# Optimization experiments

Measured on AMD Instinct MI355X. Metric: run time of the kernel, lower is better.

Reference implementation:

```python
import jax, jax.numpy as jnp
import numpy as np

D_MODEL = 1024
NUM_HEADS = 16
D_K = D_MODEL // NUM_HEADS
THETA = 10000.0


def apply_rope(x, positions):
    # x: [b, h, s, d_k]; positions: [b, s] int32
    half = D_K // 2
    inv_freq = THETA ** (-jnp.arange(half, dtype=jnp.float32) * 2.0 / D_K)  # [half]
    angles = positions[:, None, :, None].astype(jnp.float32) * inv_freq  # [b,1,s,half]
    cos, sin = jnp.cos(angles), jnp.sin(angles)
    x1 = x[..., 0::2]  # even dims
    x2 = x[..., 1::2]  # odd dims
    out_even = x1 * cos - x2 * sin
    out_odd = x1 * sin + x2 * cos
    # re-interleave
    out = jnp.stack([out_even, out_odd], axis=-1)
    return out.reshape(x.shape)


def setup_inputs() -> dict:
    key = jax.random.key(0)
    ks = jax.random.split(key, 5)
    b, s = 2, 2048
    scale = 0.02
    return {
        "x": jax.random.normal(ks[0], (b, s, D_MODEL), dtype=jnp.float32),
        "Wq": jax.random.normal(ks[1], (D_MODEL, D_MODEL), dtype=jnp.float32) * scale,
        "Wk": jax.random.normal(ks[2], (D_MODEL, D_MODEL), dtype=jnp.float32) * scale,
        "Wv": jax.random.normal(ks[3], (D_MODEL, D_MODEL), dtype=jnp.float32) * scale,
        "Wo": jax.random.normal(ks[4], (D_MODEL, D_MODEL), dtype=jnp.float32) * scale,
    }


def reference(x, Wq, Wk, Wv, Wo):
    b, s, _ = x.shape
    # Linear(d, d) applied as x @ W^T (torch Linear convention, no bias)
    Q = x @ Wq.T
    K = x @ Wk.T
    V = x @ Wv.T
    # split heads: [b, s, h*d] -> [b, h, s, d]
    split = lambda t: t.reshape(b, s, NUM_HEADS, D_K).transpose(0, 2, 1, 3)
    Q, K, V = split(Q), split(K), split(V)
    positions = jnp.broadcast_to(jnp.arange(s, dtype=jnp.int32), (b, s))
    Q = apply_rope(Q, positions)
    K = apply_rope(K, positions)
    scores = jnp.einsum('bhqd,bhkd->bhqk', Q, K) / jnp.sqrt(jnp.float32(D_K))
    causal = jnp.tril(jnp.ones((s, s), dtype=bool))
    scores = jnp.where(causal[None, None], scores, -jnp.inf)
    attn = jax.nn.softmax(scores, axis=-1)
    out = jnp.einsum('bhqk,bhkd->bhqd', attn, V)
    out = out.transpose(0, 2, 1, 3).reshape(b, s, D_MODEL)
    return out @ Wo.T
```

## Files before the change

### kernel.cpp

```cpp
#include <hip/hip_runtime.h>

typedef __attribute__((ext_vector_type(8))) short bf16x8;
typedef __attribute__((ext_vector_type(4))) float f32x4;
typedef __attribute__((ext_vector_type(16))) float f32x16;

typedef const __attribute__((address_space(1))) unsigned int gu32;
typedef __attribute__((address_space(3))) unsigned int lu32;

__device__ __forceinline__ void async16(const void* g, void* l) {
  __builtin_amdgcn_global_load_lds((gu32*)g, (lu32*)l, 16, 0, 0);
}

__device__ __forceinline__ unsigned short f2bf(float f) {
  unsigned int u = __float_as_uint(f);
  u += 0x7fffu + ((u >> 16) & 1u);
  return (unsigned short)(u >> 16);
}
__device__ __forceinline__ float b2f(unsigned short s) {
  return __uint_as_float(((unsigned int)s) << 16);
}
__device__ __forceinline__ unsigned int cvtpk(float lo, float hi) {
  unsigned int w;
  asm("v_cvt_pk_bf16_f32 %0, %1, %2" : "=v"(w) : "v"(lo), "v"(hi));
  return w;
}
__device__ __forceinline__ void plswap(unsigned int& x, unsigned int& y) {
  asm("v_permlane32_swap_b32 %0, %1" : "+v"(x), "+v"(y));
}
__device__ __forceinline__ float max3f(float a, float b, float c) {
  float d;
  asm("v_max3_f32 %0, %1, %2, %3" : "=v"(d) : "v"(a), "v"(b), "v"(c));
  return d;
}

__global__ __launch_bounds__(256) void cvt_all(const float* __restrict__ x,
                                               const float* __restrict__ Wq,
                                               const float* __restrict__ Wk,
                                               const float* __restrict__ Wv,
                                               const float* __restrict__ Wo,
                                               unsigned short* __restrict__ xb,
                                               unsigned short* __restrict__ Wb,
                                               unsigned short* __restrict__ Wob) {
  int i = blockIdx.x * 256 + threadIdx.x;
  const float* src;
  unsigned short* dst;
  int j;
  if (i < (1 << 20)) {
    src = x; dst = xb; j = i;
  } else {
    int k = i - (1 << 20);
    int wsel = k >> 18;
    j = k & 0x3FFFF;
    src = (wsel == 0) ? Wq : (wsel == 1) ? Wk : (wsel == 2) ? Wv : Wo;
    dst = (wsel == 0) ? Wb : (wsel == 1) ? Wb + (1 << 20)
        : (wsel == 2) ? Wb + (2 << 20) : Wob;
  }
  float4 v = ((const float4*)src)[j];
  ushort4 o;
  o.x = f2bf(v.x); o.y = f2bf(v.y); o.z = f2bf(v.z); o.w = f2bf(v.w);
  ((ushort4*)dst)[j] = o;
}

template <int WRITE_F32>
__global__ __launch_bounds__(256) void gemm_bt(const unsigned short* __restrict__ A,
                                               const unsigned short* __restrict__ B,
                                               void* __restrict__ Cp, int N, int K) {
  __shared__ __align__(16) unsigned short Al[3][128 * 32];
  __shared__ __align__(16) unsigned short Bl[3][128 * 32];
  const int t = threadIdx.x;
  const int w = t >> 6, l = t & 63;
  const int wm = w >> 1, wn = w & 1;
  const int lr = l & 15, lg = l >> 4;
  const long bm = (long)blockIdx.x * 128, bn = (long)blockIdx.y * 128;
  const int srow = t >> 2;
  const int c8 = t & 3;
  const int KT = K >> 5;
  f32x4 acc[4][4] = {};

  auto STAGE = [&](int ts) {
    const int bi = ts % 3;
    const int k0 = ts * 32;
    #pragma unroll
    for (int r = 0; r < 2; ++r) {
      int row = r * 64 + srow;
      async16(&A[(bm + row) * (long)K + k0 + c8 * 8], &Al[bi][row * 32 + c8 * 8]);
      async16(&B[(bn + row) * (long)K + k0 + c8 * 8], &Bl[bi][row * 32 + c8 * 8]);
    }
  };

  STAGE(0);
  STAGE(1);
  for (int kt = 0; kt < KT; ++kt) {
    const int cur = kt % 3;
    if (kt < KT - 1) asm volatile("s_waitcnt vmcnt(4)" ::: "memory");
    else             asm volatile("s_waitcnt vmcnt(0)" ::: "memory");
    __builtin_amdgcn_s_barrier();
    __builtin_amdgcn_sched_barrier(0);
    if (kt + 2 < KT) STAGE(kt + 2);
    bf16x8 af[4], bf[4];
    #pragma unroll
    for (int i = 0; i < 4; ++i) {
      af[i] = *(const bf16x8*)&Al[cur][(wm * 64 + i * 16 + lr) * 32 + lg * 8];
      bf[i] = *(const bf16x8*)&Bl[cur][(wn * 64 + i * 16 + lr) * 32 + lg * 8];
    }
    #pragma unroll
    for (int i = 0; i < 4; ++i)
      #pragma unroll
      for (int j = 0; j < 4; ++j)
        acc[i][j] = __builtin_amdgcn_mfma_f32_16x16x32_bf16(af[i], bf[j], acc[i][j], 0, 0, 0);
  }
  #pragma unroll
  for (int i = 0; i < 4; ++i)
    #pragma unroll
    for (int j = 0; j < 4; ++j)
      #pragma unroll
      for (int r = 0; r < 4; ++r) {
        long row = bm + wm * 64 + i * 16 + lg * 4 + r;
        long col = bn + wn * 64 + j * 16 + lr;
        float v = acc[i][j][r];
        if (WRITE_F32) ((float*)Cp)[row * N + col] = v;
        else ((unsigned short*)Cp)[row * N + col] = f2bf(v);
      }
}

__global__ __launch_bounds__(128) void gemm2_bt(const unsigned short* __restrict__ A,
                                                const unsigned short* __restrict__ B,
                                                float* __restrict__ Cp, int N, int K) {
  __shared__ __align__(16) unsigned short Al[3][64 * 32];
  __shared__ __align__(16) unsigned short Bl[3][128 * 32];
  const int t = threadIdx.x;
  const int w = t >> 6, l = t & 63;
  const int lr = l & 15, lg = l >> 4;
  const long bm = (long)blockIdx.x * 64, bn = (long)blockIdx.y * 128;
  const int KT = K >> 5;
  f32x4 acc[4][4] = {};

  auto STAGE = [&](int ts) {
    const int bi = ts % 3;
    const int k0 = ts * 32;
    #pragma unroll
    for (int r = 0; r < 2; ++r) {
      int u = r * 128 + 64 * w + l;
      int row = u >> 2, c8 = u & 3;
      async16(&A[(bm + row) * (long)K + k0 + c8 * 8], &Al[bi][row * 32 + c8 * 8]);
    }
    #pragma unroll
    for (int r = 0; r < 4; ++r) {
      int u = r * 128 + 64 * w + l;
      int row = u >> 2, c8 = u & 3;
      async16(&B[(bn + row) * (long)K + k0 + c8 * 8], &Bl[bi][row * 32 + c8 * 8]);
    }
  };

  STAGE(0);
  STAGE(1);
  for (int kt = 0; kt < KT; ++kt) {
    const int cur = kt % 3;
    if (kt < KT - 1) asm volatile("s_waitcnt vmcnt(6)" ::: "memory");
    else             asm volatile("s_waitcnt vmcnt(0)" ::: "memory");
    __builtin_amdgcn_s_barrier();
    __builtin_amdgcn_sched_barrier(0);
    if (kt + 2 < KT) STAGE(kt + 2);
    bf16x8 af[4], bf[4];
    #pragma unroll
    for (int i = 0; i < 4; ++i) {
      af[i] = *(const bf16x8*)&Al[cur][(i * 16 + lr) * 32 + lg * 8];
      bf[i] = *(const bf16x8*)&Bl[cur][(w * 64 + i * 16 + lr) * 32 + lg * 8];
    }
    #pragma unroll
    for (int i = 0; i < 4; ++i)
      #pragma unroll
      for (int j = 0; j < 4; ++j)
        acc[i][j] = __builtin_amdgcn_mfma_f32_16x16x32_bf16(af[i], bf[j], acc[i][j], 0, 0, 0);
  }
  #pragma unroll
  for (int i = 0; i < 4; ++i)
    #pragma unroll
    for (int j = 0; j < 4; ++j)
      #pragma unroll
      for (int r = 0; r < 4; ++r) {
        long row = bm + i * 16 + lg * 4 + r;
        long col = bn + w * 64 + j * 16 + lr;
        Cp[row * N + col] = acc[i][j][r];
      }
}

__global__ __launch_bounds__(256) void ropevtr_k(unsigned short* __restrict__ QKV,
                                                 unsigned short* __restrict__ Vt) {
  __shared__ unsigned short tl[64][66];
  const int bx = blockIdx.x;
  const int t = threadIdx.x;
  if (bx < 4096) {
    float* csl = (float*)&tl[0][0];
    float* snl = csl + 32;
    const int row = bx;
    const int s = row & 2047;
    if (t < 32) {
      float invf = exp2f((float)t * (-13.287712379549449f / 32.0f));
      float sn, cs;
      sincosf((float)s * invf, &sn, &cs);
      csl[t] = cs; snl[t] = sn;
    }
    __syncthreads();
    const int col0 = (t < 128) ? t * 8 : 1024 + (t - 128) * 8;
    const int i0 = (t & 7) * 4;
    unsigned short* p = &QKV[(size_t)row * 3072 + col0];
    bf16x8 v = *(const bf16x8*)p;
    bf16x8 o;
    #pragma unroll
    for (int j = 0; j < 4; ++j) {
      float x1 = b2f((unsigned short)v[2 * j]);
      float x2 = b2f((unsigned short)v[2 * j + 1]);
      float cs = csl[i0 + j], sn = snl[i0 + j];
      o[2 * j]     = (short)f2bf(x1 * cs - x2 * sn);
      o[2 * j + 1] = (short)f2bf(x1 * sn + x2 * cs);
    }
    *(bf16x8*)p = o;
  } else {
    const int idx = bx - 4096;
    const int kt = idx & 31;
    const int bh = idx >> 5;
    const int b = bh >> 4, h = bh & 15;
    const int row = t >> 3, c8 = t & 7;
    #pragma unroll
    for (int r = 0; r < 2; ++r) {
      int k = r * 32 + row;
      bf16x8 v = *(const bf16x8*)&QKV[((long)b * 2048 + kt * 64 + k) * 3072 + 2048 + h * 64 + c8 * 8];
      #pragma unroll
      for (int j = 0; j < 8; ++j) tl[c8 * 8 + j][k] = (unsigned short)v[j];
    }
    __syncthreads();
    #pragma unroll
    for (int r = 0; r < 2; ++r) {
      int d = r * 32 + row;
      ushort4 a, bq;
      a.x = tl[d][c8 * 8 + 0]; a.y = tl[d][c8 * 8 + 1];
      a.z = tl[d][c8 * 8 + 2]; a.w = tl[d][c8 * 8 + 3];
      bq.x = tl[d][c8 * 8 + 4]; bq.y = tl[d][c8 * 8 + 5];
      bq.z = tl[d][c8 * 8 + 6]; bq.w = tl[d][c8 * 8 + 7];
      long off = ((long)bh * 64 + d) * 2048 + kt * 64 + c8 * 8;
      *(ushort4*)&Vt[off] = a;
      *(ushort4*)&Vt[off + 4] = bq;
    }
  }
}

__global__ __launch_bounds__(256) void attn_k(const unsigned short* __restrict__ QKV,
                                              const unsigned short* __restrict__ VtG,
                                              unsigned short* __restrict__ O) {
  __shared__ __align__(16) unsigned short Kl[3][64 * 64];
  __shared__ __align__(16) unsigned short Vl[3][64 * 64];
  const int t = threadIdx.x;
  const int w = t >> 6, l = t & 63;
  const int q31 = l & 31, hi = l >> 5;
  const int bh = blockIdx.x;
  const int y = (int)blockIdx.y;
  const int qt = (y < 8) ? (15 - y) : (y - 8);
  const int b = bh >> 4, h = bh & 15;
  const int Qb = qt * 128;
  const long rowb = (long)b * 2048;
  const int L = 3072;
  const int NT = 2 * qt + 2;
  const float cexp = 0.125f * 1.4426950408889634f;

  const int qmy = Qb + 32 * w + q31;
  const long qgrow = rowb + qmy;
  const int ktmax = (Qb + 32 * w) >> 6;

  bf16x8 qf[4];
  #pragma unroll
  for (int dk = 0; dk < 4; ++dk)
    qf[dk] = *(const bf16x8*)&QKV[qgrow * L + h * 64 + dk * 16 + hi * 8];

  bf16x8 onesf;
  #pragma unroll
  for (int j = 0; j < 8; ++j) onesf[j] = (short)0x3F80;

  float m_ = -1e30f;
  f32x16 oa[2], la;
  #pragma unroll
  for (int r = 0; r < 16; ++r) { oa[0][r] = 0.0f; oa[1][r] = 0.0f; la[r] = 0.0f; }

  auto STAGE = [&](int ts) {
    const int bi = ts % 3;
    const long kb = rowb + (long)ts * 64;
    const long vrowb = (long)bh * 64;
    #pragma unroll
    for (int r = 0; r < 2; ++r) {
      int row = w * 16 + r * 8 + (l >> 3);
      int c8s = ((l & 7) ^ (row & 7)) * 8;
      async16(&QKV[(kb + row) * L + 1024 + h * 64 + c8s], &Kl[bi][row * 64 + (l & 7) * 8]);
      async16(&VtG[(vrowb + row) * 2048 + ts * 64 + c8s], &Vl[bi][row * 64 + (l & 7) * 8]);
    }
  };

  auto QK = [&](f32x16 (&st)[2], int bi) {
    #pragma unroll
    for (int kt2 = 0; kt2 < 2; ++kt2)
      #pragma unroll
      for (int r = 0; r < 16; ++r) st[kt2][r] = 0.0f;
    __builtin_amdgcn_s_setprio(1);
    #pragma unroll
    for (int dk = 0; dk < 4; ++dk)
      #pragma unroll
      for (int kt2 = 0; kt2 < 2; ++kt2) {
        int krow = kt2 * 32 + q31;
        bf16x8 kfr = *(const bf16x8*)&Kl[bi][krow * 64 + (((2 * dk + hi) ^ (krow & 7)) * 8)];
        st[kt2] = __builtin_amdgcn_mfma_f32_32x32x16_bf16(kfr, qf[dk], st[kt2], 0, 0, 0);
      }
    __builtin_amdgcn_s_setprio(0);
  };

  auto SMPV = [&](f32x16 (&st)[2], int kt) {
    if (kt == ktmax) {
      #pragma unroll
      for (int kt2 = 0; kt2 < 2; ++kt2)
        #pragma unroll
        for (int r = 0; r < 16; ++r) {
          int kg = kt * 64 + kt2 * 32 + (r & 3) + 8 * (r >> 2) + 4 * hi;
          if (kg > qmy) st[kt2][r] = -1e30f;
        }
    }
    float m0[8];
    #pragma unroll
    for (int i = 0; i < 8; ++i)
      m0[i] = max3f(st[0][i], st[0][i + 8], fmaxf(st[1][i], st[1][i + 8]));
    float mt = max3f(max3f(m0[0], m0[1], m0[2]), max3f(m0[3], m0[4], m0[5]),
                     fmaxf(m0[6], m0[7]));
    if (__any((mt - m_) * cexp > 8.0f)) {
      float mg = fmaxf(mt, __shfl_xor(mt, 32, 64));
      float mn = fmaxf(m_, mg);
      float al = __builtin_amdgcn_exp2f((m_ - mn) * cexp);
      m_ = mn;
      la[0] *= al;
      #pragma unroll
      for (int dt = 0; dt < 2; ++dt)
        #pragma unroll
        for (int r = 0; r < 16; ++r) oa[dt][r] *= al;
    }
    const float mc = m_ * cexp;
    #pragma unroll
    for (int kt2 = 0; kt2 < 2; ++kt2)
      #pragma unroll
      for (int r = 0; r < 16; ++r)
        st[kt2][r] = __builtin_amdgcn_exp2f(fmaf(st[kt2][r], cexp, -mc));
    bf16x8 pfr[4];
    #pragma unroll
    for (int ks = 0; ks < 4; ++ks) {
      int tt = ks >> 1, gX = 2 * (ks & 1), gY = gX + 1;
      unsigned int x1 = cvtpk(st[tt][4 * gX + 0], st[tt][4 * gX + 1]);
      unsigned int y1 = cvtpk(st[tt][4 * gY + 0], st[tt][4 * gY + 1]);
      plswap(x1, y1);
      unsigned int x2 = cvtpk(st[tt][4 * gX + 2], st[tt][4 * gX + 3]);
      unsigned int y2 = cvtpk(st[tt][4 * gY + 2], st[tt][4 * gY + 3]);
      plswap(x2, y2);
      union { unsigned int u[4]; bf16x8 b; } cc;
      cc.u[0] = x1; cc.u[1] = x2; cc.u[2] = y1; cc.u[3] = y2;
      pfr[ks] = cc.b;
    }
    const int vb = kt % 3;
    __builtin_amdgcn_s_setprio(1);
    #pragma unroll
    for (int ks = 0; ks < 4; ++ks) {
      la = __builtin_amdgcn_mfma_f32_32x32x16_bf16(onesf, pfr[ks], la, 0, 0, 0);
      #pragma unroll
      for (int dt = 0; dt < 2; ++dt) {
        int vrow = dt * 32 + q31;
        bf16x8 vf = *(const bf16x8*)&Vl[vb][vrow * 64 + (((2 * ks + hi) ^ (vrow & 7)) * 8)];
        oa[dt] = __builtin_amdgcn_mfma_f32_32x32x16_bf16(vf, pfr[ks], oa[dt], 0, 0, 0);
      }
    }
    __builtin_amdgcn_s_setprio(0);
  };

  f32x16 stA[2], stB[2];

  STAGE(0);
  STAGE(1);
  asm volatile("s_waitcnt vmcnt(4)" ::: "memory");
  __builtin_amdgcn_s_barrier();
  __builtin_amdgcn_sched_barrier(0);
  QK(stA, 0);

  auto STEP = [&](f32x16 (&cur)[2], f32x16 (&nxt)[2], int kt) {
    asm volatile("s_waitcnt vmcnt(0)" ::: "memory");
    __builtin_amdgcn_s_barrier();
    __builtin_amdgcn_sched_barrier(0);
    if (kt + 1 < NT && kt + 1 <= ktmax) QK(nxt, (kt + 1) % 3);
    if (kt + 2 < NT) STAGE(kt + 2);
    if (kt <= ktmax) SMPV(cur, kt);
  };

  int kt = 0;
  while (kt < NT) {
    STEP(stA, stB, kt); ++kt;
    if (kt < NT) { STEP(stB, stA, kt); ++kt; }
  }

  float inv = 1.0f / la[0];
  #pragma unroll
  for (int dt = 0; dt < 2; ++dt)
    #pragma unroll
    for (int g = 0; g < 4; ++g) {
      ushort4 o4;
      o4.x = f2bf(oa[dt][4 * g + 0] * inv);
      o4.y = f2bf(oa[dt][4 * g + 1] * inv);
      o4.z = f2bf(oa[dt][4 * g + 2] * inv);
      o4.w = f2bf(oa[dt][4 * g + 3] * inv);
      *(ushort4*)&O[qgrow * 1024 + h * 64 + dt * 32 + 8 * g + 4 * hi] = o4;
    }
}

extern "C" void kernel_launch(void* const* d_in, const int* in_sizes, int n_in,
                              void* d_out, int out_size, void* d_ws, size_t ws_size,
                              hipStream_t stream) {
  const float* x  = (const float*)d_in[0];
  const float* Wq = (const float*)d_in[1];
  const float* Wk = (const float*)d_in[2];
  const float* Wv = (const float*)d_in[3];
  const float* Wo = (const float*)d_in[4];
  char* ws = (char*)d_ws;
  unsigned short* xb   = (unsigned short*)(ws);
  unsigned short* Wb   = (unsigned short*)(ws + (8u << 20));
  unsigned short* Wob  = (unsigned short*)(ws + (14u << 20));
  unsigned short* QKVb = (unsigned short*)(ws + (16u << 20));
  unsigned short* Ob   = (unsigned short*)(ws + (40u << 20));
  unsigned short* Vtg  = xb;

  cvt_all<<<8192, 256, 0, stream>>>(x, Wq, Wk, Wv, Wo, xb, Wb, Wob);
  gemm_bt<0><<<dim3(32, 24), 256, 0, stream>>>(xb, Wb, QKVb, 3072, 1024);
  ropevtr_k<<<5120, 256, 0, stream>>>(QKVb, Vtg);
  attn_k<<<dim3(32, 16), 256, 0, stream>>>(QKVb, Vtg, Ob);
  gemm2_bt<<<dim3(64, 8), 128, 0, stream>>>(Ob, Wob, (float*)d_out, 1024, 1024);
}
```

Measured before the change: 123.3 us.

## Process keys in 128-wide double-buffered superblocks instead of a pipelined 64-key ring

```diff
diff --git a/kernel.cpp b/kernel.cpp
--- a/kernel.cpp
+++ b/kernel.cpp
@@ -248,8 +248,8 @@
 __global__ __launch_bounds__(256) void attn_k(const unsigned short* __restrict__ QKV,
                                               const unsigned short* __restrict__ VtG,
                                               unsigned short* __restrict__ O) {
-  __shared__ __align__(16) unsigned short Kl[3][64 * 64];
-  __shared__ __align__(16) unsigned short Vl[3][64 * 64];
+  __shared__ __align__(16) unsigned short Kl[2][2][64 * 64];
+  __shared__ __align__(16) unsigned short Vl[2][2][64 * 64];
   const int t = threadIdx.x;
   const int w = t >> 6, l = t & 63;
   const int q31 = l & 31, hi = l >> 5;
@@ -260,7 +260,7 @@
   const int Qb = qt * 128;
   const long rowb = (long)b * 2048;
   const int L = 3072;
-  const int NT = 2 * qt + 2;
+  const int NTS = qt + 1;
   const float cexp = 0.125f * 1.4426950408889634f;
 
   const int qmy = Qb + 32 * w + q31;
@@ -281,50 +281,70 @@
   #pragma unroll
   for (int r = 0; r < 16; ++r) { oa[0][r] = 0.0f; oa[1][r] = 0.0f; la[r] = 0.0f; }
 
-  auto STAGE = [&](int ts) {
-    const int bi = ts % 3;
-    const long kb = rowb + (long)ts * 64;
+  auto STAGE2 = [&](int ts) {
+    const int bi = ts & 1;
     const long vrowb = (long)bh * 64;
     #pragma unroll
-    for (int r = 0; r < 2; ++r) {
-      int row = w * 16 + r * 8 + (l >> 3);
-      int c8s = ((l & 7) ^ (row & 7)) * 8;
-      async16(&QKV[(kb + row) * L + 1024 + h * 64 + c8s], &Kl[bi][row * 64 + (l & 7) * 8]);
-      async16(&VtG[(vrowb + row) * 2048 + ts * 64 + c8s], &Vl[bi][row * 64 + (l & 7) * 8]);
+    for (int s = 0; s < 2; ++s) {
+      const int kt = 2 * ts + s;
+      const long kb = rowb + (long)kt * 64;
+      #pragma unroll
+      for (int r = 0; r < 2; ++r) {
+        int row = w * 16 + r * 8 + (l >> 3);
+        int c8s = ((l & 7) ^ (row & 7)) * 8;
+        async16(&QKV[(kb + row) * L + 1024 + h * 64 + c8s], &Kl[bi][s][row * 64 + (l & 7) * 8]);
+        async16(&VtG[(vrowb + row) * 2048 + kt * 64 + c8s], &Vl[bi][s][row * 64 + (l & 7) * 8]);
+      }
     }
   };
 
-  auto QK = [&](f32x16 (&st)[2], int bi) {
-    #pragma unroll
-    for (int kt2 = 0; kt2 < 2; ++kt2)
-      #pragma unroll
-      for (int r = 0; r < 16; ++r) st[kt2][r] = 0.0f;
+  STAGE2(0);
+
+  for (int ts = 0; ts < NTS; ++ts) {
+    const int bi = ts & 1;
+    asm volatile("s_waitcnt vmcnt(0)" ::: "memory");
+    __builtin_amdgcn_s_barrier();
+    __builtin_amdgcn_sched_barrier(0);
+    if (ts + 1 < NTS) STAGE2(ts + 1);
+
+    f32x16 st[2][2];
+    #pragma unroll
+    for (int s = 0; s < 2; ++s)
+      #pragma unroll
+      for (int kt2 = 0; kt2 < 2; ++kt2)
+        #pragma unroll
+        for (int r = 0; r < 16; ++r) st[s][kt2][r] = 0.0f;
     __builtin_amdgcn_s_setprio(1);
     #pragma unroll
     for (int dk = 0; dk < 4; ++dk)
       #pragma unroll
-      for (int kt2 = 0; kt2 < 2; ++kt2) {
-        int krow = kt2 * 32 + q31;
-        bf16x8 kfr = *(const bf16x8*)&Kl[bi][krow * 64 + (((2 * dk + hi) ^ (krow & 7)) * 8)];
-        st[kt2] = __builtin_amdgcn_mfma_f32_32x32x16_bf16(kfr, qf[dk], st[kt2], 0, 0, 0);
-      }
+      for (int s = 0; s < 2; ++s)
+        #pragma unroll
+        for (int kt2 = 0; kt2 < 2; ++kt2) {
+          int krow = kt2 * 32 + q31;
+          bf16x8 kfr = *(const bf16x8*)&Kl[bi][s][krow * 64 + (((2 * dk + hi) ^ (krow & 7)) * 8)];
+          st[s][kt2] = __builtin_amdgcn_mfma_f32_32x32x16_bf16(kfr, qf[dk], st[s][kt2], 0, 0, 0);
+        }
     __builtin_amdgcn_s_setprio(0);
-  };
-
-  auto SMPV = [&](f32x16 (&st)[2], int kt) {
-    if (kt == ktmax) {
-      #pragma unroll
-      for (int kt2 = 0; kt2 < 2; ++kt2)
-        #pragma unroll
-        for (int r = 0; r < 16; ++r) {
-          int kg = kt * 64 + kt2 * 32 + (r & 3) + 8 * (r >> 2) + 4 * hi;
-          if (kg > qmy) st[kt2][r] = -1e30f;
-        }
+    #pragma unroll
+    for (int s = 0; s < 2; ++s) {
+      int kt = 2 * ts + s;
+      if (kt >= ktmax) {
+        #pragma unroll
+        for (int kt2 = 0; kt2 < 2; ++kt2)
+          #pragma unroll
+          for (int r = 0; r < 16; ++r) {
+            int kg = kt * 64 + kt2 * 32 + (r & 3) + 8 * (r >> 2) + 4 * hi;
+            if (kg > qmy) st[s][kt2][r] = -1e30f;
+          }
+      }
     }
     float m0[8];
     #pragma unroll
     for (int i = 0; i < 8; ++i)
-      m0[i] = max3f(st[0][i], st[0][i + 8], fmaxf(st[1][i], st[1][i + 8]));
+      m0[i] = fmaxf(fmaxf(max3f(st[0][0][i], st[0][0][i + 8], st[0][1][i]),
+                          max3f(st[0][1][i + 8], st[1][0][i], st[1][0][i + 8])),
+                    fmaxf(st[1][1][i], st[1][1][i + 8]));
     float mt = max3f(max3f(m0[0], m0[1], m0[2]), max3f(m0[3], m0[4], m0[5]),
                      fmaxf(m0[6], m0[7]));
     if (__any((mt - m_) * cexp > 8.0f)) {
@@ -340,61 +360,41 @@
     }
     const float mc = m_ * cexp;
     #pragma unroll
-    for (int kt2 = 0; kt2 < 2; ++kt2)
-      #pragma unroll
-      for (int r = 0; r < 16; ++r)
-        st[kt2][r] = __builtin_amdgcn_exp2f(fmaf(st[kt2][r], cexp, -mc));
-    bf16x8 pfr[4];
-    #pragma unroll
-    for (int ks = 0; ks < 4; ++ks) {
-      int tt = ks >> 1, gX = 2 * (ks & 1), gY = gX + 1;
-      unsigned int x1 = cvtpk(st[tt][4 * gX + 0], st[tt][4 * gX + 1]);
-      unsigned int y1 = cvtpk(st[tt][4 * gY + 0], st[tt][4 * gY + 1]);
-      plswap(x1, y1);
-      unsigned int x2 = cvtpk(st[tt][4 * gX + 2], st[tt][4 * gX + 3]);
-      unsigned int y2 = cvtpk(st[tt][4 * gY + 2], st[tt][4 * gY + 3]);
-      plswap(x2, y2);
-      union { unsigned int u[4]; bf16x8 b; } cc;
-      cc.u[0] = x1; cc.u[1] = x2; cc.u[2] = y1; cc.u[3] = y2;
-      pfr[ks] = cc.b;
-    }
-    const int vb = kt % 3;
-    __builtin_amdgcn_s_setprio(1);
-    #pragma unroll
-    for (int ks = 0; ks < 4; ++ks) {
-      la = __builtin_amdgcn_mfma_f32_32x32x16_bf16(onesf, pfr[ks], la, 0, 0, 0);
-      #pragma unroll
-      for (int dt = 0; dt < 2; ++dt) {
-        int vrow = dt * 32 + q31;
-        bf16x8 vf = *(const bf16x8*)&Vl[vb][vrow * 64 + (((2 * ks + hi) ^ (vrow & 7)) * 8)];
-        oa[dt] = __builtin_amdgcn_mfma_f32_32x32x16_bf16(vf, pfr[ks], oa[dt], 0, 0, 0);
-      }
-    }
-    __builtin_amdgcn_s_setprio(0);
-  };
-
-  f32x16 stA[2], stB[2];
-
-  STAGE(0);
-  STAGE(1);
-  asm volatile("s_waitcnt vmcnt(4)" ::: "memory");
-  __builtin_amdgcn_s_barrier();
-  __builtin_amdgcn_sched_barrier(0);
-  QK(stA, 0);
-
-  auto STEP = [&](f32x16 (&cur)[2], f32x16 (&nxt)[2], int kt) {
-    asm volatile("s_waitcnt vmcnt(0)" ::: "memory");
-    __builtin_amdgcn_s_barrier();
-    __builtin_amdgcn_sched_barrier(0);
-    if (kt + 1 < NT && kt + 1 <= ktmax) QK(nxt, (kt + 1) % 3);
-    if (kt + 2 < NT) STAGE(kt + 2);
-    if (kt <= ktmax) SMPV(cur, kt);
-  };
-
-  int kt = 0;
-  while (kt < NT) {
-    STEP(stA, stB, kt); ++kt;
-    if (kt < NT) { STEP(stB, stA, kt); ++kt; }
+    for (int s = 0; s < 2; ++s)
+      #pragma unroll
+      for (int kt2 = 0; kt2 < 2; ++kt2)
+        #pragma unroll
+        for (int r = 0; r < 16; ++r)
+          st[s][kt2][r] = __builtin_amdgcn_exp2f(fmaf(st[s][kt2][r], cexp, -mc));
+    #pragma unroll
+    for (int s = 0; s < 2; ++s) {
+      bf16x8 pfr[4];
+      #pragma unroll
+      for (int ks = 0; ks < 4; ++ks) {
+        int tt = ks >> 1, gX = 2 * (ks & 1), gY = gX + 1;
+        unsigned int x1 = cvtpk(st[s][tt][4 * gX + 0], st[s][tt][4 * gX + 1]);
+        unsigned int y1 = cvtpk(st[s][tt][4 * gY + 0], st[s][tt][4 * gY + 1]);
+        plswap(x1, y1);
+        unsigned int x2 = cvtpk(st[s][tt][4 * gX + 2], st[s][tt][4 * gX + 3]);
+        unsigned int y2 = cvtpk(st[s][tt][4 * gY + 2], st[s][tt][4 * gY + 3]);
+        plswap(x2, y2);
+        union { unsigned int u[4]; bf16x8 b; } cc;
+        cc.u[0] = x1; cc.u[1] = x2; cc.u[2] = y1; cc.u[3] = y2;
+        pfr[ks] = cc.b;
+      }
+      __builtin_amdgcn_s_setprio(1);
+      #pragma unroll
+      for (int ks = 0; ks < 4; ++ks) {
+        la = __builtin_amdgcn_mfma_f32_32x32x16_bf16(onesf, pfr[ks], la, 0, 0, 0);
+        #pragma unroll
+        for (int dt = 0; dt < 2; ++dt) {
+          int vrow = dt * 32 + q31;
+          bf16x8 vf = *(const bf16x8*)&Vl[bi][s][vrow * 64 + (((2 * ks + hi) ^ (vrow & 7)) * 8)];
+          oa[dt] = __builtin_amdgcn_mfma_f32_32x32x16_bf16(vf, pfr[ks], oa[dt], 0, 0, 0);
+        }
+      }
+      __builtin_amdgcn_s_setprio(0);
+    }
   }
 
   float inv = 1.0f / la[0];
```

Result: no change. 121.6 us (median of 15 runs) (-1.4%).
